# Optimization experiments

Measured on AMD Instinct MI355X. Metric: run time of the kernel, lower is better.

The kernel has to match this reference:

```python
import jax, jax.numpy as jnp
import numpy as np

COMMITMENT_COST = 0.25


def setup_inputs() -> dict:
    key = jax.random.key(0)
    k1, k2 = jax.random.split(key)
    B, S, D, V = 4, 1024, 1024, 32002
    inputs_embeds = jax.random.normal(k1, (B, S, D), dtype=jnp.float32)
    emb_weight = jax.random.normal(k2, (V, D), dtype=jnp.float32)
    attention_mask = jnp.ones((B, S), dtype=jnp.float32)
    return {
        "inputs_embeds": inputs_embeds,
        "emb_weight": emb_weight,
        "attention_mask": attention_mask,
        "lab_seq_len": 9,
    }


def reference(inputs_embeds, emb_weight, attention_mask, lab_seq_len):
    V, D = emb_weight.shape
    qn = (V - 2) // (lab_seq_len - 1)          # codes per segment
    nseg = lab_seq_len - 1                      # number of segments (V-2 divisible by qn)
    # codebook segments, skipping 2 special tokens: (nseg, qn, D)
    codes = emb_weight[2:2 + nseg * qn].reshape(nseg, qn, D)

    x = inputs_embeds.reshape(-1, D)            # (N, D)
    x2 = jnp.sum(x * x, axis=1)                 # (N,)
    c2 = jnp.sum(codes * codes, axis=-1)        # (nseg, qn)
    dots = jnp.einsum("nd,sqd->nsq", x, codes)  # (N, nseg, qn)
    dist = x2[:, None, None] + c2[None] - 2.0 * dots

    idx = jnp.argmin(dist, axis=-1)             # (N, nseg)
    # gather selected code per segment: (N, nseg, D)
    sel = codes[jnp.arange(nseg)[None, :], idx]
    # sum over segments then divide by segment count (matches torch loop + /j)
    quantized = jnp.mean(sel, axis=1).reshape(inputs_embeds.shape)

    mask = attention_mask[..., None]
    mse = jnp.mean((quantized * mask - inputs_embeds * mask) ** 2)
    # e_latent_loss and q_latent_loss are identical in the source
    loss = mse + COMMITMENT_COST * mse

    quantized_st = inputs_embeds + jax.lax.stop_gradient(quantized - inputs_embeds)
    return quantized_st, loss
```

## Files before the change

kernel.cpp:

```cpp
#include <hip/hip_runtime.h>
#include <stdint.h>

#define D_DIM  1024
#define NROWS  4096
#define NSEG   8
#define QN     4000
#define NCODES 32000
#define VOFF   2

#define BM 256
#define BN 256
#define BKI 128
#define LDK 40

#define MARGIN_BF 2.0f
#define MARGIN_I8 6.0f
#define CAP      262144u

#define C2_OFF     0u
#define X2_OFF     131072u
#define CELLS_OFF  147456u
#define MINF_OFF   409600u
#define CNT_OFF    540672u
#define PART_OFF   540928u
#define LIST_OFF   573696u
#define STASH_OFF  1622272u
#define WS_NEED_A  10010880u
#define XI8_OFF    10010880u
#define CI8_OFF    14205184u
#define SX_OFF     46973184u
#define SC_OFF     46989568u
#define WS_NEED_FAST 83935488u

typedef short bf16x8 __attribute__((ext_vector_type(8)));
typedef float f32x4  __attribute__((ext_vector_type(4)));
typedef int   i32x4  __attribute__((ext_vector_type(4)));

#define AS1(p) ((const __attribute__((address_space(1))) void*)(p))
#define AS3(p) ((__attribute__((address_space(3))) void*)(p))

__device__ inline unsigned short f2bs(float f) {
  unsigned u = __float_as_uint(f);
  unsigned r = (u + 0x7FFFu + ((u >> 16) & 1u)) >> 16;
  return (unsigned short)r;
}
__device__ inline unsigned shflx_u32(unsigned v, int m) {
  return (unsigned)__shfl_xor((int)v, m, 64);
}
__device__ inline unsigned packkey(float d, int qloc) {
  return (__float_as_uint(fmaxf(d, 0.0f)) & 0xFFFFFF80u) | (unsigned)qloc;
}

__global__ __launch_bounds__(256) void rowsq_kernel(const float* __restrict__ emb,
                                                    const float* __restrict__ x,
                                                    float* __restrict__ c2,
                                                    float* __restrict__ x2) {
  int b = blockIdx.x;
  int t = threadIdx.x;
  const float* src = (b < NCODES) ? (emb + (size_t)(VOFF + b) * D_DIM)
                                  : (x + (size_t)(b - NCODES) * D_DIM);
  float4 v = ((const float4*)src)[t];
  float s = v.x * v.x + v.y * v.y + v.z * v.z + v.w * v.w;
  for (int off = 32; off > 0; off >>= 1) s += __shfl_down(s, off, 64);
  __shared__ float red[4];
  if ((t & 63) == 0) red[t >> 6] = s;
  __syncthreads();
  if (t == 0) {
    float tot = red[0] + red[1] + red[2] + red[3];
    if (b < NCODES) c2[b] = tot; else x2[b - NCODES] = tot;
  }
}

__global__ __launch_bounds__(256) void convert_i8_kernel(const float* __restrict__ emb,
                                                         const float* __restrict__ x,
                                                         char* __restrict__ ci8,
                                                         char* __restrict__ xi8,
                                                         float* __restrict__ c2,
                                                         float* __restrict__ x2,
                                                         float* __restrict__ scs,
                                                         float* __restrict__ sxs) {
  int b = blockIdx.x;
  int t = threadIdx.x;
  const float* src;
  char* dst;
  if (b < NCODES) { src = emb + (size_t)(VOFF + b) * D_DIM; dst = ci8 + (size_t)b * D_DIM; }
  else            { src = x + (size_t)(b - NCODES) * D_DIM; dst = xi8 + (size_t)(b - NCODES) * D_DIM; }
  float4 v = ((const float4*)src)[t];
  float s = v.x * v.x + v.y * v.y + v.z * v.z + v.w * v.w;
  float a = fmaxf(fmaxf(fabsf(v.x), fabsf(v.y)), fmaxf(fabsf(v.z), fabsf(v.w)));
  for (int off = 32; off > 0; off >>= 1) {
    s += __shfl_down(s, off, 64);
    a = fmaxf(a, __shfl_down(a, off, 64));
  }
  __shared__ float redS[4], redA[4];
  if ((t & 63) == 0) { redS[t >> 6] = s; redA[t >> 6] = a; }
  __syncthreads();
  float amax = fmaxf(fmaxf(redA[0], redA[1]), fmaxf(redA[2], redA[3]));
  float inv = (amax > 0.0f) ? (127.0f / amax) : 0.0f;
  char4 o;
  o.x = (char)__float2int_rn(v.x * inv);
  o.y = (char)__float2int_rn(v.y * inv);
  o.z = (char)__float2int_rn(v.z * inv);
  o.w = (char)__float2int_rn(v.w * inv);
  ((char4*)dst)[t] = o;
  if (t == 0) {
    float tot = redS[0] + redS[1] + redS[2] + redS[3];
    float scale = amax * (1.0f / 127.0f);
    if (b < NCODES) { c2[b] = tot; scs[b] = scale; }
    else            { x2[b - NCODES] = tot; sxs[b - NCODES] = scale; }
  }
}

__global__ __launch_bounds__(512, 2) void score_i8_kernel(
    const char* __restrict__ xi8, const char* __restrict__ ci8,
    const float* __restrict__ c2, const float* __restrict__ x2,
    const float* __restrict__ scs, const float* __restrict__ sxs,
    unsigned* __restrict__ stash) {
  __shared__ char lA[2][BM][BKI];
  __shared__ char lB[2][BN][BKI];
  int tid = threadIdx.x;

  int bid = ((blockIdx.x & 7) << 8) | (blockIdx.x >> 3);
  int seg = bid >> 8;
  int lb  = bid & 255;
  int g   = lb >> 4;
  int gi  = lb & 15;
  int mx  = (g & 3) * 4 + (gi & 3);
  int qy  = (g >> 2) * 4 + (gi >> 2);
  int m0 = mx * BM, q0 = qy * BN;

  int lane = tid & 63, wid = tid >> 6;
  int wr = wid & 3, wc = wid >> 2;
  int lrow = lane & 15, kg = lane >> 4;
  const int co0 = ((kg       ^ (lrow & 7)) << 4);
  const int co1 = (((4 | kg) ^ (lrow & 7)) << 4);

  int csh = (((tid & 7) ^ ((tid >> 3) & 7)) << 4);
  const char* aSt = xi8 + (size_t)(m0 + (tid >> 3)) * D_DIM + csh;
  const char* bSt0; const char* bSt1; const char* bSt2; const char* bSt3;
  {
    int r0 = q0 +   0 + (tid >> 3); if (r0 > QN - 1) r0 = QN - 1;
    int r1 = q0 +  64 + (tid >> 3); if (r1 > QN - 1) r1 = QN - 1;
    int r2 = q0 + 128 + (tid >> 3); if (r2 > QN - 1) r2 = QN - 1;
    int r3 = q0 + 192 + (tid >> 3); if (r3 > QN - 1) r3 = QN - 1;
    bSt0 = ci8 + (size_t)(seg * QN + r0) * D_DIM + csh;
    bSt1 = ci8 + (size_t)(seg * QN + r1) * D_DIM + csh;
    bSt2 = ci8 + (size_t)(seg * QN + r2) * D_DIM + csh;
    bSt3 = ci8 + (size_t)(seg * QN + r3) * D_DIM + csh;
  }
  int ldsOff = tid << 4;

  i32x4 aR[2][2];
  i32x4 bR[4][2];
  i32x4 acc[4][8];
#pragma unroll
  for (int i = 0; i < 4; i++)
#pragma unroll
    for (int j = 0; j < 8; j++) acc[i][j] = (i32x4){0, 0, 0, 0};

#define STAGE_A(bb, kt) {                                                                      \
    __builtin_amdgcn_global_load_lds(AS1(aSt + (size_t)  0 * D_DIM + (kt)), AS3(&lA[bb][  0][0] + ldsOff), 16, 0, 0); \
    __builtin_amdgcn_global_load_lds(AS1(aSt + (size_t) 64 * D_DIM + (kt)), AS3(&lA[bb][ 64][0] + ldsOff), 16, 0, 0); \
    __builtin_amdgcn_global_load_lds(AS1(aSt + (size_t)128 * D_DIM + (kt)), AS3(&lA[bb][128][0] + ldsOff), 16, 0, 0); \
    __builtin_amdgcn_global_load_lds(AS1(aSt + (size_t)192 * D_DIM + (kt)), AS3(&lA[bb][192][0] + ldsOff), 16, 0, 0); }
#define STAGE_B(bb, kt) {                                                                      \
    __builtin_amdgcn_global_load_lds(AS1(bSt0 + (kt)), AS3(&lB[bb][  0][0] + ldsOff), 16, 0, 0); \
    __builtin_amdgcn_global_load_lds(AS1(bSt1 + (kt)), AS3(&lB[bb][ 64][0] + ldsOff), 16, 0, 0); \
    __builtin_amdgcn_global_load_lds(AS1(bSt2 + (kt)), AS3(&lB[bb][128][0] + ldsOff), 16, 0, 0); \
    __builtin_amdgcn_global_load_lds(AS1(bSt3 + (kt)), AS3(&lB[bb][192][0] + ldsOff), 16, 0, 0); }

#define READ_A(bb, mh) { _Pragma("unroll")                                         \
    for (int i = 0; i < 2; i++) {                                                  \
      const char* pa = &lA[bb][wr * 64 + (mh) * 32 + i * 16 + lrow][0];            \
      aR[i][0] = *(const i32x4*)(pa + co0);                                        \
      aR[i][1] = *(const i32x4*)(pa + co1); } }
#define READ_B(bb, nh) { _Pragma("unroll")                                         \
    for (int j = 0; j < 4; j++) {                                                  \
      const char* pb = &lB[bb][wc * 128 + (nh) * 64 + j * 16 + lrow][0];           \
      bR[j][0] = *(const i32x4*)(pb + co0);                                        \
      bR[j][1] = *(const i32x4*)(pb + co1); } }

#define MFMA_Q(mh, nh) {                                                           \
    __builtin_amdgcn_s_setprio(1);                                                 \
    _Pragma("unroll") for (int ks = 0; ks < 2; ks++)                               \
      _Pragma("unroll") for (int i = 0; i < 2; i++)                                \
        _Pragma("unroll") for (int j = 0; j < 4; j++)                              \
          acc[(mh)*2 + i][(nh)*4 + j] = __builtin_amdgcn_mfma_i32_16x16x64_i8(     \
              aR[i][ks], bR[j][ks], acc[(mh)*2 + i][(nh)*4 + j], 0, 0, 0);         \
    __builtin_amdgcn_s_setprio(0); }

#define VM0   asm volatile("s_waitcnt vmcnt(0)" ::: "memory")
#define LGKM0 asm volatile("s_waitcnt lgkmcnt(0)" ::: "memory")
#define BARX  __builtin_amdgcn_s_barrier()

  STAGE_A(0, 0);
  STAGE_B(0, 0);
  VM0; BARX;

  int buf = 0;
  for (int t = 0; t < 8; ++t) {
    int ktn = (t + 1) << 7;
    READ_A(buf, 0); READ_B(buf, 0);
    if (t < 7) STAGE_A(buf ^ 1, ktn);
    BARX; LGKM0; MFMA_Q(0, 0); BARX;
    READ_A(buf, 1);
    if (t < 7) STAGE_B(buf ^ 1, ktn);
    BARX; LGKM0; MFMA_Q(1, 0); BARX;
    READ_B(buf, 1);
    BARX; LGKM0; MFMA_Q(1, 1); BARX;
    READ_A(buf, 0);
    BARX; LGKM0; MFMA_Q(0, 1);
    VM0; LGKM0; BARX;
    buf ^= 1;
  }

  float c2v[8], s2c[8];
  bool  val[8];
#pragma unroll
  for (int nf = 0; nf < 8; nf++) {
    int q = q0 + wc * 128 + nf * 16 + lrow;
    val[nf] = (q < QN);
    int qc = val[nf] ? q : QN - 1;
    c2v[nf] = c2[seg * QN + qc];
    s2c[nf] = 2.0f * scs[seg * QN + qc];
  }

#pragma unroll
  for (int mf = 0; mf < 4; mf++) {
#pragma unroll
    for (int r = 0; r < 4; r++) {
      int grow = m0 + wr * 64 + mf * 16 + kg * 4 + r;
      float x2r = x2[grow];
      float sxr = sxs[grow];
      unsigned b1 = 0xFFFFFFFFu, b2 = 0xFFFFFFFFu;
#pragma unroll
      for (int nf = 0; nf < 8; nf++) {
        unsigned u = 0xFFFFFFFFu;
        if (val[nf]) {
          float d = (x2r + c2v[nf]) - sxr * s2c[nf] * (float)acc[mf][nf][r];
          u = packkey(d, nf * 16 + lrow);
        }
        if (u < b1) { b2 = b1; b1 = u; } else if (u < b2) b2 = u;
      }
#pragma unroll
      for (int m = 1; m < 16; m <<= 1) {
        unsigned o1 = shflx_u32(b1, m), o2 = shflx_u32(b2, m);
        unsigned n1 = min(b1, o1);
        unsigned n2 = min(max(b1, o1), min(b2, o2));
        b1 = n1; b2 = n2;
      }
      if (lrow == 0) {
        size_t base = ((size_t)(grow * NSEG + seg) * 32 + (qy * 2 + wc)) * 2;
        stash[base + 0] = b1;
        stash[base + 1] = b2;
      }
    }
  }
#undef STAGE_A
#undef STAGE_B
#undef READ_A
#undef READ_B
#undef MFMA_Q
#undef VM0
#undef LGKM0
#undef BARX
}

template<int MODE>
__global__ __launch_bounds__(256) void score_mfma_kernel(
    const float* __restrict__ x, const float* __restrict__ emb,
    const float* __restrict__ c2, const float* __restrict__ x2,
    unsigned* __restrict__ minf, unsigned* __restrict__ stash,
    unsigned* __restrict__ list, unsigned* __restrict__ cnt) {
  __shared__ short lA[2][128][LDK];
  __shared__ short lB[2][128][LDK];
  int tid = threadIdx.x;
  int m0 = blockIdx.x * 128, q0 = blockIdx.y * 128, seg = blockIdx.z;
  int lane = tid & 63, wid = tid >> 6;
  int wr = wid >> 1, wc = wid & 1;
  int lrow = lane & 15, kg = lane >> 4;

  int sr = tid >> 1;
  int kh = (tid & 1) << 4;
  const float* abase = x + (size_t)(m0 + sr) * D_DIM + kh;
  int qg = q0 + sr; if (qg > QN - 1) qg = QN - 1;
  const float* bbase = emb + (size_t)(VOFF + seg * QN + qg) * D_DIM + kh;

  f32x4 acc[4][4];
#pragma unroll
  for (int i = 0; i < 4; i++)
#pragma unroll
    for (int j = 0; j < 4; j++) acc[i][j] = (f32x4){0.f, 0.f, 0.f, 0.f};

  float4 ra0, ra1, ra2, ra3, rb0, rb1, rb2, rb3;

#define LOAD_TILE(kt) {                                          \
    const float4* ap = (const float4*)(abase + (kt));            \
    const float4* bp = (const float4*)(bbase + (kt));            \
    ra0 = ap[0]; ra1 = ap[1]; ra2 = ap[2]; ra3 = ap[3];          \
    rb0 = bp[0]; rb1 = bp[1]; rb2 = bp[2]; rb3 = bp[3]; }

#define WRITE_TILE(bb) {                                                       \
    bf16x8 p0, p1, q0v, q1v;                                                   \
    p0[0]=f2bs(ra0.x); p0[1]=f2bs(ra0.y); p0[2]=f2bs(ra0.z); p0[3]=f2bs(ra0.w);\
    p0[4]=f2bs(ra1.x); p0[5]=f2bs(ra1.y); p0[6]=f2bs(ra1.z); p0[7]=f2bs(ra1.w);\
    p1[0]=f2bs(ra2.x); p1[1]=f2bs(ra2.y); p1[2]=f2bs(ra2.z); p1[3]=f2bs(ra2.w);\
    p1[4]=f2bs(ra3.x); p1[5]=f2bs(ra3.y); p1[6]=f2bs(ra3.z); p1[7]=f2bs(ra3.w);\
    q0v[0]=f2bs(rb0.x); q0v[1]=f2bs(rb0.y); q0v[2]=f2bs(rb0.z); q0v[3]=f2bs(rb0.w);\
    q0v[4]=f2bs(rb1.x); q0v[5]=f2bs(rb1.y); q0v[6]=f2bs(rb1.z); q0v[7]=f2bs(rb1.w);\
    q1v[0]=f2bs(rb2.x); q1v[1]=f2bs(rb2.y); q1v[2]=f2bs(rb2.z); q1v[3]=f2bs(rb2.w);\
    q1v[4]=f2bs(rb3.x); q1v[5]=f2bs(rb3.y); q1v[6]=f2bs(rb3.z); q1v[7]=f2bs(rb3.w);\
    *(bf16x8*)&lA[bb][sr][kh]     = p0;  *(bf16x8*)&lA[bb][sr][kh + 8] = p1;   \
    *(bf16x8*)&lB[bb][sr][kh]     = q0v; *(bf16x8*)&lB[bb][sr][kh + 8] = q1v; }

#define COMPUTE(bb) {                                                              \
    bf16x8 af0 = *(const bf16x8*)&lA[bb][wr * 64 +  0 + lrow][kg * 8];             \
    bf16x8 af1 = *(const bf16x8*)&lA[bb][wr * 64 + 16 + lrow][kg * 8];             \
    bf16x8 af2 = *(const bf16x8*)&lA[bb][wr * 64 + 32 + lrow][kg * 8];             \
    bf16x8 af3 = *(const bf16x8*)&lA[bb][wr * 64 + 48 + lrow][kg * 8];             \
    bf16x8 bg0 = *(const bf16x8*)&lB[bb][wc * 64 +  0 + lrow][kg * 8];             \
    bf16x8 bg1 = *(const bf16x8*)&lB[bb][wc * 64 + 16 + lrow][kg * 8];             \
    bf16x8 bg2 = *(const bf16x8*)&lB[bb][wc * 64 + 32 + lrow][kg * 8];             \
    bf16x8 bg3 = *(const bf16x8*)&lB[bb][wc * 64 + 48 + lrow][kg * 8];             \
    acc[0][0] = __builtin_amdgcn_mfma_f32_16x16x32_bf16(af0, bg0, acc[0][0],0,0,0);\
    acc[0][1] = __builtin_amdgcn_mfma_f32_16x16x32_bf16(af0, bg1, acc[0][1],0,0,0);\
    acc[0][2] = __builtin_amdgcn_mfma_f32_16x16x32_bf16(af0, bg2, acc[0][2],0,0,0);\
    acc[0][3] = __builtin_amdgcn_mfma_f32_16x16x32_bf16(af0, bg3, acc[0][3],0,0,0);\
    acc[1][0] = __builtin_amdgcn_mfma_f32_16x16x32_bf16(af1, bg0, acc[1][0],0,0,0);\
    acc[1][1] = __builtin_amdgcn_mfma_f32_16x16x32_bf16(af1, bg1, acc[1][1],0,0,0);\
    acc[1][2] = __builtin_amdgcn_mfma_f32_16x16x32_bf16(af1, bg2, acc[1][2],0,0,0);\
    acc[1][3] = __builtin_amdgcn_mfma_f32_16x16x32_bf16(af1, bg3, acc[1][3],0,0,0);\
    acc[2][0] = __builtin_amdgcn_mfma_f32_16x16x32_bf16(af2, bg0, acc[2][0],0,0,0);\
    acc[2][1] = __builtin_amdgcn_mfma_f32_16x16x32_bf16(af2, bg1, acc[2][1],0,0,0);\
    acc[2][2] = __builtin_amdgcn_mfma_f32_16x16x32_bf16(af2, bg2, acc[2][2],0,0,0);\
    acc[2][3] = __builtin_amdgcn_mfma_f32_16x16x32_bf16(af2, bg3, acc[2][3],0,0,0);\
    acc[3][0] = __builtin_amdgcn_mfma_f32_16x16x32_bf16(af3, bg0, acc[3][0],0,0,0);\
    acc[3][1] = __builtin_amdgcn_mfma_f32_16x16x32_bf16(af3, bg1, acc[3][1],0,0,0);\
    acc[3][2] = __builtin_amdgcn_mfma_f32_16x16x32_bf16(af3, bg2, acc[3][2],0,0,0);\
    acc[3][3] = __builtin_amdgcn_mfma_f32_16x16x32_bf16(af3, bg3, acc[3][3],0,0,0); }

  LOAD_TILE(0);
  WRITE_TILE(0);
  __syncthreads();
  int buf = 0;
  for (int kt = 32; kt < D_DIM; kt += 32) {
    LOAD_TILE(kt);
    COMPUTE(buf);
    WRITE_TILE(buf ^ 1);
    __syncthreads();
    buf ^= 1;
  }
  COMPUTE(buf);
  unsigned* mbuf = (unsigned*)&lA[0][0][0];

  float c2v[4];
  bool  val[4];
  int   qloc[4];
#pragma unroll
  for (int nt = 0; nt < 4; nt++) {
    int ql = wc * 64 + nt * 16 + lrow;
    int q = q0 + ql;
    val[nt] = (q < QN);
    qloc[nt] = ql;
    c2v[nt] = c2[seg * QN + (val[nt] ? q : QN - 1)];
  }

#pragma unroll
  for (int mt = 0; mt < 4; mt++) {
#pragma unroll
    for (int r = 0; r < 4; r++) {
      int grow = m0 + wr * 64 + mt * 16 + kg * 4 + r;
      float x2r = x2[grow];
      if constexpr (MODE == 0) {
        float dmin = 1e30f;
#pragma unroll
        for (int nt = 0; nt < 4; nt++) {
          if (val[nt]) {
            float d = (x2r + c2v[nt]) - 2.0f * acc[mt][nt][r];
            dmin = fminf(dmin, d);
          }
        }
        dmin = fminf(dmin, __shfl_xor(dmin, 1, 64));
        dmin = fminf(dmin, __shfl_xor(dmin, 2, 64));
        dmin = fminf(dmin, __shfl_xor(dmin, 4, 64));
        dmin = fminf(dmin, __shfl_xor(dmin, 8, 64));
        if (lrow == 0)
          atomicMin(&minf[grow * NSEG + seg], __float_as_uint(fmaxf(dmin, 0.0f)));
      } else if constexpr (MODE == 1) {
        unsigned b1 = 0xFFFFFFFFu, b2 = 0xFFFFFFFFu;
#pragma unroll
        for (int nt = 0; nt < 4; nt++) {
          unsigned u = 0xFFFFFFFFu;
          if (val[nt]) {
            float d = (x2r + c2v[nt]) - 2.0f * acc[mt][nt][r];
            u = packkey(d, qloc[nt]);
          }
          if (u < b1) { b2 = b1; b1 = u; } else if (u < b2) b2 = u;
        }
#pragma unroll
        for (int m = 1; m < 16; m <<= 1) {
          unsigned o1 = shflx_u32(b1, m), o2 = shflx_u32(b2, m);
          unsigned n1 = min(b1, o1);
          unsigned n2 = min(max(b1, o1), min(b2, o2));
          b1 = n1; b2 = n2;
        }
        if (lrow == 0) {
          int rloc = wr * 64 + mt * 16 + kg * 4 + r;
          mbuf[(rloc * 2 + wc) * 2 + 0] = b1;
          mbuf[(rloc * 2 + wc) * 2 + 1] = b2;
        }
      } else {
        float dm = __uint_as_float(minf[grow * NSEG + seg]) + MARGIN_BF;
#pragma unroll
        for (int nt = 0; nt < 4; nt++) {
          if (val[nt]) {
            float d = (x2r + c2v[nt]) - 2.0f * acc[mt][nt][r];
            if (d <= dm) {
              unsigned idx = atomicAdd(cnt, 1u);
              if (idx < CAP)
                list[idx] = ((unsigned)grow << 15) | ((unsigned)seg << 12) |
                            (unsigned)(q0 + qloc[nt]);
            }
          }
        }
      }
    }
  }

  if constexpr (MODE == 1) {
    __syncthreads();
    if (tid < 128) {
      unsigned p1 = mbuf[(tid * 2 + 0) * 2 + 0];
      unsigned p2 = mbuf[(tid * 2 + 0) * 2 + 1];
      unsigned g1 = mbuf[(tid * 2 + 1) * 2 + 0];
      unsigned g2 = mbuf[(tid * 2 + 1) * 2 + 1];
      unsigned m1 = min(p1, g1);
      unsigned m2 = min(max(p1, g1), min(p2, g2));
      int grow = m0 + tid;
      size_t base = ((size_t)(grow * NSEG + seg) * 32 + blockIdx.y) * 2;
      stash[base + 0] = m1;
      stash[base + 1] = m2;
    }
  }
#undef LOAD_TILE
#undef WRITE_TILE
#undef COMPUTE
}

__global__ __launch_bounds__(256) void filter_rescore_kernel(
    const float* __restrict__ x, const float* __restrict__ emb,
    const float* __restrict__ c2, const float* __restrict__ x2,
    const unsigned* __restrict__ stash, unsigned long long* __restrict__ cells,
    float margin) {
  int cell = blockIdx.x * 4 + (threadIdx.x >> 6);
  int lane = threadIdx.x & 63;
  int row = cell >> 3, seg = cell & 7;
  unsigned e = stash[(size_t)cell * 64 + lane];
  unsigned m = e;
  for (int msk = 1; msk < 64; msk <<= 1) m = min(m, shflx_u32(m, msk));
  float dcut = __uint_as_float(m & 0xFFFFFF80u) + margin;
  int myq = ((lane >> 1) << 7) + (int)(e & 127u);
  bool qual = (e != 0xFFFFFFFFu) &&
              (__uint_as_float(e & 0xFFFFFF80u) <= dcut) && (myq < QN);
  unsigned long long mask = __ballot(qual);
  unsigned long long best = 0ULL;
  const float4* xr = (const float4*)(x + (size_t)row * D_DIM);
  float x2r = x2[row];
  while (mask) {
    int L = __ffsll((long long)mask) - 1;
    mask &= mask - 1;
    int q = __shfl(myq, L, 64);
    const float4* cr = (const float4*)(emb + (size_t)(VOFF + seg * QN + q) * D_DIM);
    float s = 0.f;
#pragma unroll
    for (int j = 0; j < 4; j++) {
      float4 a = xr[j * 64 + lane];
      float4 b = cr[j * 64 + lane];
      s += a.x * b.x + a.y * b.y + a.z * b.z + a.w * b.w;
    }
    for (int msk2 = 1; msk2 < 64; msk2 <<= 1) s += __shfl_xor(s, msk2, 64);
    float dist = (x2r + c2[seg * QN + q]) - 2.0f * s;
    unsigned u = __float_as_uint(dist);
    unsigned asc = (u & 0x80000000u) ? ~u : (u | 0x80000000u);
    unsigned long long p = ((unsigned long long)(~asc) << 32) |
                           (unsigned long long)(~(unsigned)q);
    if (p > best) best = p;
  }
  if (lane == 0) cells[(size_t)row * NSEG + seg] = best;
}

__global__ __launch_bounds__(256) void rescore_kernel(const float* __restrict__ x,
                                                      const float* __restrict__ emb,
                                                      const float* __restrict__ c2,
                                                      const float* __restrict__ x2,
                                                      const unsigned* __restrict__ list,
                                                      const unsigned* __restrict__ cnt,
                                                      unsigned long long* __restrict__ cells) {
  int nw = gridDim.x * 4;
  int wv = blockIdx.x * 4 + (threadIdx.x >> 6);
  int lane = threadIdx.x & 63;
  unsigned n = *cnt; if (n > CAP) n = CAP;
  for (unsigned i = wv; i < n; i += nw) {
    unsigned e = list[i];
    int row = e >> 15, seg = (e >> 12) & 7, q = e & 4095;
    const float4* xr = (const float4*)(x + (size_t)row * D_DIM);
    const float4* cr = (const float4*)(emb + (size_t)(VOFF + seg * QN + q) * D_DIM);
    float s = 0.f;
#pragma unroll
    for (int j = 0; j < 4; j++) {
      float4 a = xr[j * 64 + lane];
      float4 b = cr[j * 64 + lane];
      s += a.x * b.x + a.y * b.y + a.z * b.z + a.w * b.w;
    }
    for (int msk = 1; msk < 64; msk <<= 1) s += __shfl_xor(s, msk, 64);
    float dist = (x2[row] + c2[seg * QN + q]) - 2.0f * s;
    unsigned u = __float_as_uint(dist);
    unsigned asc = (u & 0x80000000u) ? ~u : (u | 0x80000000u);
    unsigned long long p = ((unsigned long long)(~asc) << 32) |
                           (unsigned long long)(~(unsigned)q);
    if (lane == 0) atomicMax(&cells[(size_t)row * NSEG + seg], p);
  }
}

__global__ __launch_bounds__(256) void gather_kernel(const float* __restrict__ x,
                                                     const float* __restrict__ emb,
                                                     const float* __restrict__ mask,
                                                     const unsigned long long* __restrict__ cells,
                                                     float* __restrict__ out,
                                                     double* __restrict__ part) {
  int n = blockIdx.x;
  int t = threadIdx.x;
  __shared__ int qsel[NSEG];
  if (t < NSEG) qsel[t] = (int)(~(unsigned)(cells[(size_t)n * NSEG + t] & 0xffffffffULL));
  __syncthreads();
  float4 xv = ((const float4*)(x + (size_t)n * D_DIM))[t];
  float ax = 0.f, ay = 0.f, az = 0.f, aw = 0.f;
#pragma unroll
  for (int s = 0; s < NSEG; s++) {
    float4 cv = ((const float4*)(emb + (size_t)(VOFF + s * QN + qsel[s]) * D_DIM))[t];
    ax += cv.x; ay += cv.y; az += cv.z; aw += cv.w;
  }
  float qx = ax * 0.125f, qy = ay * 0.125f, qz = az * 0.125f, qw = aw * 0.125f;
  float4 o4;
  o4.x = xv.x + (qx - xv.x);
  o4.y = xv.y + (qy - xv.y);
  o4.z = xv.z + (qz - xv.z);
  o4.w = xv.w + (qw - xv.w);
  ((float4*)(out + (size_t)n * D_DIM))[t] = o4;
  float mk = mask[n];
  float dx = qx * mk - xv.x * mk;
  float dy = qy * mk - xv.y * mk;
  float dz = qz * mk - xv.z * mk;
  float dw = qw * mk - xv.w * mk;
  float ss = dx * dx + dy * dy + dz * dz + dw * dw;
  double sd = (double)ss;
  for (int off = 32; off > 0; off >>= 1) sd += __shfl_down(sd, off, 64);
  __shared__ double red[4];
  if ((t & 63) == 0) red[t >> 6] = sd;
  __syncthreads();
  if (t == 0) part[n] = red[0] + red[1] + red[2] + red[3];
}

__global__ __launch_bounds__(256) void finalize_kernel(const double* __restrict__ part,
                                                       float* __restrict__ loss_out) {
  int t = threadIdx.x;
  double s = 0.0;
  for (int i = t; i < NROWS; i += 256) s += part[i];
  for (int off = 32; off > 0; off >>= 1) s += __shfl_down(s, off, 64);
  __shared__ double red[4];
  if ((t & 63) == 0) red[t >> 6] = s;
  __syncthreads();
  if (t == 0) {
    double tot = red[0] + red[1] + red[2] + red[3];
    float m = (float)(tot / (double)((size_t)NROWS * D_DIM));
    loss_out[0] = m + 0.25f * m;
  }
}

extern "C" void kernel_launch(void* const* d_in, const int* in_sizes, int n_in,
                              void* d_out, int out_size, void* d_ws, size_t ws_size,
                              hipStream_t stream) {
  const float* x    = (const float*)d_in[0];
  const float* emb  = (const float*)d_in[1];
  const float* mask = (const float*)d_in[2];
  (void)in_sizes; (void)n_in; (void)out_size;

  char* ws = (char*)d_ws;
  float* c2 = (float*)(ws + C2_OFF);
  float* x2 = (float*)(ws + X2_OFF);
  unsigned long long* cells = (unsigned long long*)(ws + CELLS_OFF);
  unsigned* minf = (unsigned*)(ws + MINF_OFF);
  unsigned* cnt  = (unsigned*)(ws + CNT_OFF);
  double*   part = (double*)(ws + PART_OFF);
  unsigned* list = (unsigned*)(ws + LIST_OFF);
  unsigned* stash = (unsigned*)(ws + STASH_OFF);
  char* xi8 = ws + XI8_OFF;
  char* ci8 = ws + CI8_OFF;
  float* sxs = (float*)(ws + SX_OFF);
  float* scs = (float*)(ws + SC_OFF);
  float* out = (float*)d_out;

  hipMemsetAsync(cells, 0, 262144, stream);
  hipMemsetAsync(cnt, 0, 256, stream);

  if (ws_size >= (size_t)WS_NEED_FAST) {
    convert_i8_kernel<<<dim3(NCODES + NROWS), 256, 0, stream>>>(emb, x, ci8, xi8, c2, x2, scs, sxs);
    score_i8_kernel<<<dim3(2048), 512, 0, stream>>>(xi8, ci8, c2, x2, scs, sxs, stash);
    filter_rescore_kernel<<<dim3(8192), 256, 0, stream>>>(x, emb, c2, x2, stash, cells, MARGIN_I8);
    gather_kernel<<<dim3(NROWS), 256, 0, stream>>>(x, emb, mask, cells, out, part);
  } else if (ws_size >= (size_t)WS_NEED_A) {
    rowsq_kernel<<<dim3(NCODES + NROWS), 256, 0, stream>>>(emb, x, c2, x2);
    score_mfma_kernel<1><<<dim3(NROWS / 128, (QN + 127) / 128, NSEG), 256, 0, stream>>>(
        x, emb, c2, x2, minf, stash, list, cnt);
    filter_rescore_kernel<<<dim3(8192), 256, 0, stream>>>(x, emb, c2, x2, stash, cells, MARGIN_BF);
    gather_kernel<<<dim3(NROWS), 256, 0, stream>>>(x, emb, mask, cells, out, part);
  } else {
    hipMemsetAsync(minf, 0xFF, 131072, stream);
    rowsq_kernel<<<dim3(NCODES + NROWS), 256, 0, stream>>>(emb, x, c2, x2);
    score_mfma_kernel<0><<<dim3(NROWS / 128, (QN + 127) / 128, NSEG), 256, 0, stream>>>(
        x, emb, c2, x2, minf, stash, list, cnt);
    score_mfma_kernel<2><<<dim3(NROWS / 128, (QN + 127) / 128, NSEG), 256, 0, stream>>>(
        x, emb, c2, x2, minf, stash, list, cnt);
    rescore_kernel<<<dim3(2048), 256, 0, stream>>>(x, emb, c2, x2, list, cnt, cells);
    gather_kernel<<<dim3(NROWS), 256, 0, stream>>>(x, emb, mask, cells, out, part);
  }
  finalize_kernel<<<dim3(1), 256, 0, stream>>>(part, out + (size_t)NROWS * D_DIM);
}
```

Measured before the change: 282.6 us.

## Retile int8 scoring GEMM to 128x128 blocks with triple-buffered K pipeline

The int8 distance-scoring kernel moves from 256x256 tiles with 512 threads and double buffering to 128x128 tiles with 256 threads, K steps of 64, and a three-stage global-to-LDS pipeline using partial vmcnt waits. The per-block top-2 results from the two wave columns are merged in shared memory before writing one stash entry per row, so the stash indexing changes to 32 column blocks of 128. The aim is better occupancy and load/compute overlap, at the cost of less data reuse per tile and four times as many blocks.

```diff
diff --git a/kernel.cpp b/kernel.cpp
--- a/kernel.cpp
+++ b/kernel.cpp
@@ -8,9 +8,6 @@
 #define NCODES 32000
 #define VOFF   2
 
-#define BM 256
-#define BN 256
-#define BKI 128
 #define LDK 40
 
 #define MARGIN_BF 2.0f
@@ -111,134 +108,128 @@
   }
 }
 
-__global__ __launch_bounds__(512, 2) void score_i8_kernel(
+__global__ __launch_bounds__(256) void score_i8_kernel(
     const char* __restrict__ xi8, const char* __restrict__ ci8,
     const float* __restrict__ c2, const float* __restrict__ x2,
     const float* __restrict__ scs, const float* __restrict__ sxs,
     unsigned* __restrict__ stash) {
-  __shared__ char lA[2][BM][BKI];
-  __shared__ char lB[2][BN][BKI];
+  __shared__ char lA[3][128][64];
+  __shared__ char lB[3][128][64];
   int tid = threadIdx.x;
 
-  int bid = ((blockIdx.x & 7) << 8) | (blockIdx.x >> 3);
-  int seg = bid >> 8;
-  int lb  = bid & 255;
-  int g   = lb >> 4;
-  int gi  = lb & 15;
-  int mx  = (g & 3) * 4 + (gi & 3);
-  int qy  = (g >> 2) * 4 + (gi >> 2);
-  int m0 = mx * BM, q0 = qy * BN;
+  int bid = ((blockIdx.x & 7) << 10) | (blockIdx.x >> 3);
+  int lb  = bid & 63;
+  int sb  = bid >> 6;
+  int smx = sb & 3;
+  int sqy = (sb >> 2) & 3;
+  int seg = sb >> 4;
+  int mx  = smx * 8 + (lb & 7);
+  int qy  = sqy * 8 + (lb >> 3);
+  int m0 = mx * 128, q0 = qy * 128;
 
   int lane = tid & 63, wid = tid >> 6;
-  int wr = wid & 3, wc = wid >> 2;
+  int wr = wid >> 1, wc = wid & 1;
   int lrow = lane & 15, kg = lane >> 4;
-  const int co0 = ((kg       ^ (lrow & 7)) << 4);
-  const int co1 = (((4 | kg) ^ (lrow & 7)) << 4);
-
-  int csh = (((tid & 7) ^ ((tid >> 3) & 7)) << 4);
-  const char* aSt = xi8 + (size_t)(m0 + (tid >> 3)) * D_DIM + csh;
-  const char* bSt0; const char* bSt1; const char* bSt2; const char* bSt3;
-  {
-    int r0 = q0 +   0 + (tid >> 3); if (r0 > QN - 1) r0 = QN - 1;
-    int r1 = q0 +  64 + (tid >> 3); if (r1 > QN - 1) r1 = QN - 1;
-    int r2 = q0 + 128 + (tid >> 3); if (r2 > QN - 1) r2 = QN - 1;
-    int r3 = q0 + 192 + (tid >> 3); if (r3 > QN - 1) r3 = QN - 1;
-    bSt0 = ci8 + (size_t)(seg * QN + r0) * D_DIM + csh;
-    bSt1 = ci8 + (size_t)(seg * QN + r1) * D_DIM + csh;
-    bSt2 = ci8 + (size_t)(seg * QN + r2) * D_DIM + csh;
-    bSt3 = ci8 + (size_t)(seg * QN + r3) * D_DIM + csh;
-  }
+  const int co = ((kg ^ ((lrow >> 1) & 3)) << 4);
+
+  int srow = tid >> 2;
+  int scol = (((tid & 3) ^ ((tid >> 3) & 3)) << 4);
+  const char* aSrc0 = xi8 + (size_t)(m0 + srow) * D_DIM + scol;
+  const char* aSrc1 = aSrc0 + (size_t)64 * D_DIM;
+  int qb0 = q0 + srow;      if (qb0 > QN - 1) qb0 = QN - 1;
+  int qb1 = q0 + srow + 64; if (qb1 > QN - 1) qb1 = QN - 1;
+  const char* bSrc0 = ci8 + (size_t)(seg * QN + qb0) * D_DIM + scol;
+  const char* bSrc1 = ci8 + (size_t)(seg * QN + qb1) * D_DIM + scol;
   int ldsOff = tid << 4;
 
-  i32x4 aR[2][2];
-  i32x4 bR[4][2];
-  i32x4 acc[4][8];
+  i32x4 acc[4][4];
 #pragma unroll
   for (int i = 0; i < 4; i++)
 #pragma unroll
-    for (int j = 0; j < 8; j++) acc[i][j] = (i32x4){0, 0, 0, 0};
-
-#define STAGE_A(bb, kt) {                                                                      \
-    __builtin_amdgcn_global_load_lds(AS1(aSt + (size_t)  0 * D_DIM + (kt)), AS3(&lA[bb][  0][0] + ldsOff), 16, 0, 0); \
-    __builtin_amdgcn_global_load_lds(AS1(aSt + (size_t) 64 * D_DIM + (kt)), AS3(&lA[bb][ 64][0] + ldsOff), 16, 0, 0); \
-    __builtin_amdgcn_global_load_lds(AS1(aSt + (size_t)128 * D_DIM + (kt)), AS3(&lA[bb][128][0] + ldsOff), 16, 0, 0); \
-    __builtin_amdgcn_global_load_lds(AS1(aSt + (size_t)192 * D_DIM + (kt)), AS3(&lA[bb][192][0] + ldsOff), 16, 0, 0); }
-#define STAGE_B(bb, kt) {                                                                      \
-    __builtin_amdgcn_global_load_lds(AS1(bSt0 + (kt)), AS3(&lB[bb][  0][0] + ldsOff), 16, 0, 0); \
-    __builtin_amdgcn_global_load_lds(AS1(bSt1 + (kt)), AS3(&lB[bb][ 64][0] + ldsOff), 16, 0, 0); \
-    __builtin_amdgcn_global_load_lds(AS1(bSt2 + (kt)), AS3(&lB[bb][128][0] + ldsOff), 16, 0, 0); \
-    __builtin_amdgcn_global_load_lds(AS1(bSt3 + (kt)), AS3(&lB[bb][192][0] + ldsOff), 16, 0, 0); }
-
-#define READ_A(bb, mh) { _Pragma("unroll")                                         \
-    for (int i = 0; i < 2; i++) {                                                  \
-      const char* pa = &lA[bb][wr * 64 + (mh) * 32 + i * 16 + lrow][0];            \
-      aR[i][0] = *(const i32x4*)(pa + co0);                                        \
-      aR[i][1] = *(const i32x4*)(pa + co1); } }
-#define READ_B(bb, nh) { _Pragma("unroll")                                         \
-    for (int j = 0; j < 4; j++) {                                                  \
-      const char* pb = &lB[bb][wc * 128 + (nh) * 64 + j * 16 + lrow][0];           \
-      bR[j][0] = *(const i32x4*)(pb + co0);                                        \
-      bR[j][1] = *(const i32x4*)(pb + co1); } }
-
-#define MFMA_Q(mh, nh) {                                                           \
+    for (int j = 0; j < 4; j++) acc[i][j] = (i32x4){0, 0, 0, 0};
+
+#define STAGE_F(bb, kt) {                                                            \
+    __builtin_amdgcn_global_load_lds(AS1(aSrc0 + (kt)), AS3(&lA[bb][0][0]  + ldsOff), 16, 0, 0); \
+    __builtin_amdgcn_global_load_lds(AS1(aSrc1 + (kt)), AS3(&lA[bb][64][0] + ldsOff), 16, 0, 0); \
+    __builtin_amdgcn_global_load_lds(AS1(bSrc0 + (kt)), AS3(&lB[bb][0][0]  + ldsOff), 16, 0, 0); \
+    __builtin_amdgcn_global_load_lds(AS1(bSrc1 + (kt)), AS3(&lB[bb][64][0] + ldsOff), 16, 0, 0); }
+
+#define COMPUTE_F(bb) {                                                            \
+    i32x4 af0 = *(const i32x4*)&lA[bb][wr * 64 +  0 + lrow][co];                   \
+    i32x4 af1 = *(const i32x4*)&lA[bb][wr * 64 + 16 + lrow][co];                   \
+    i32x4 af2 = *(const i32x4*)&lA[bb][wr * 64 + 32 + lrow][co];                   \
+    i32x4 af3 = *(const i32x4*)&lA[bb][wr * 64 + 48 + lrow][co];                   \
+    i32x4 bg0 = *(const i32x4*)&lB[bb][wc * 64 +  0 + lrow][co];                   \
+    i32x4 bg1 = *(const i32x4*)&lB[bb][wc * 64 + 16 + lrow][co];                   \
+    i32x4 bg2 = *(const i32x4*)&lB[bb][wc * 64 + 32 + lrow][co];                   \
+    i32x4 bg3 = *(const i32x4*)&lB[bb][wc * 64 + 48 + lrow][co];                   \
     __builtin_amdgcn_s_setprio(1);                                                 \
-    _Pragma("unroll") for (int ks = 0; ks < 2; ks++)                               \
-      _Pragma("unroll") for (int i = 0; i < 2; i++)                                \
-        _Pragma("unroll") for (int j = 0; j < 4; j++)                              \
-          acc[(mh)*2 + i][(nh)*4 + j] = __builtin_amdgcn_mfma_i32_16x16x64_i8(     \
-              aR[i][ks], bR[j][ks], acc[(mh)*2 + i][(nh)*4 + j], 0, 0, 0);         \
+    acc[0][0] = __builtin_amdgcn_mfma_i32_16x16x64_i8(af0, bg0, acc[0][0],0,0,0);  \
+    acc[0][1] = __builtin_amdgcn_mfma_i32_16x16x64_i8(af0, bg1, acc[0][1],0,0,0);  \
+    acc[0][2] = __builtin_amdgcn_mfma_i32_16x16x64_i8(af0, bg2, acc[0][2],0,0,0);  \
+    acc[0][3] = __builtin_amdgcn_mfma_i32_16x16x64_i8(af0, bg3, acc[0][3],0,0,0);  \
+    acc[1][0] = __builtin_amdgcn_mfma_i32_16x16x64_i8(af1, bg0, acc[1][0],0,0,0);  \
+    acc[1][1] = __builtin_amdgcn_mfma_i32_16x16x64_i8(af1, bg1, acc[1][1],0,0,0);  \
+    acc[1][2] = __builtin_amdgcn_mfma_i32_16x16x64_i8(af1, bg2, acc[1][2],0,0,0);  \
+    acc[1][3] = __builtin_amdgcn_mfma_i32_16x16x64_i8(af1, bg3, acc[1][3],0,0,0);  \
+    acc[2][0] = __builtin_amdgcn_mfma_i32_16x16x64_i8(af2, bg0, acc[2][0],0,0,0);  \
+    acc[2][1] = __builtin_amdgcn_mfma_i32_16x16x64_i8(af2, bg1, acc[2][1],0,0,0);  \
+    acc[2][2] = __builtin_amdgcn_mfma_i32_16x16x64_i8(af2, bg2, acc[2][2],0,0,0);  \
+    acc[2][3] = __builtin_amdgcn_mfma_i32_16x16x64_i8(af2, bg3, acc[2][3],0,0,0);  \
+    acc[3][0] = __builtin_amdgcn_mfma_i32_16x16x64_i8(af3, bg0, acc[3][0],0,0,0);  \
+    acc[3][1] = __builtin_amdgcn_mfma_i32_16x16x64_i8(af3, bg1, acc[3][1],0,0,0);  \
+    acc[3][2] = __builtin_amdgcn_mfma_i32_16x16x64_i8(af3, bg2, acc[3][2],0,0,0);  \
+    acc[3][3] = __builtin_amdgcn_mfma_i32_16x16x64_i8(af3, bg3, acc[3][3],0,0,0);  \
     __builtin_amdgcn_s_setprio(0); }
 
+#define VM4   asm volatile("s_waitcnt vmcnt(4)" ::: "memory")
 #define VM0   asm volatile("s_waitcnt vmcnt(0)" ::: "memory")
 #define LGKM0 asm volatile("s_waitcnt lgkmcnt(0)" ::: "memory")
 #define BARX  __builtin_amdgcn_s_barrier()
 
-  STAGE_A(0, 0);
-  STAGE_B(0, 0);
-  VM0; BARX;
-
-  int buf = 0;
-  for (int t = 0; t < 8; ++t) {
-    int ktn = (t + 1) << 7;
-    READ_A(buf, 0); READ_B(buf, 0);
-    if (t < 7) STAGE_A(buf ^ 1, ktn);
-    BARX; LGKM0; MFMA_Q(0, 0); BARX;
-    READ_A(buf, 1);
-    if (t < 7) STAGE_B(buf ^ 1, ktn);
-    BARX; LGKM0; MFMA_Q(1, 0); BARX;
-    READ_B(buf, 1);
-    BARX; LGKM0; MFMA_Q(1, 1); BARX;
-    READ_A(buf, 0);
-    BARX; LGKM0; MFMA_Q(0, 1);
-    VM0; LGKM0; BARX;
-    buf ^= 1;
-  }
-
-  float c2v[8], s2c[8];
-  bool  val[8];
-#pragma unroll
-  for (int nf = 0; nf < 8; nf++) {
-    int q = q0 + wc * 128 + nf * 16 + lrow;
-    val[nf] = (q < QN);
-    int qc = val[nf] ? q : QN - 1;
-    c2v[nf] = c2[seg * QN + qc];
-    s2c[nf] = 2.0f * scs[seg * QN + qc];
-  }
-
-#pragma unroll
-  for (int mf = 0; mf < 4; mf++) {
+  STAGE_F(0, 0);
+  STAGE_F(1, 64);
+  for (int tt = 0; tt < 12; tt += 3) {
+    VM4; LGKM0; BARX; STAGE_F(2, (tt + 2) * 64); COMPUTE_F(0);
+    VM4; LGKM0; BARX; STAGE_F(0, (tt + 3) * 64); COMPUTE_F(1);
+    VM4; LGKM0; BARX; STAGE_F(1, (tt + 4) * 64); COMPUTE_F(2);
+  }
+  VM4; LGKM0; BARX; STAGE_F(2, 14 * 64); COMPUTE_F(0);
+  VM4; LGKM0; BARX; STAGE_F(0, 15 * 64); COMPUTE_F(1);
+  VM4; LGKM0; BARX; COMPUTE_F(2);
+  VM0; LGKM0; BARX; COMPUTE_F(0);
+  __syncthreads();
+
+  unsigned* mbuf = (unsigned*)&lA[1][0][0];
+
+  float c2v[4], s2c[4];
+  bool  val[4];
+  int   qloc[4];
+#pragma unroll
+  for (int nt = 0; nt < 4; nt++) {
+    int ql = wc * 64 + nt * 16 + lrow;
+    int q = q0 + ql;
+    val[nt] = (q < QN);
+    qloc[nt] = ql;
+    int qc = val[nt] ? q : QN - 1;
+    c2v[nt] = c2[seg * QN + qc];
+    s2c[nt] = 2.0f * scs[seg * QN + qc];
+  }
+
+#pragma unroll
+  for (int mt = 0; mt < 4; mt++) {
 #pragma unroll
     for (int r = 0; r < 4; r++) {
-      int grow = m0 + wr * 64 + mf * 16 + kg * 4 + r;
+      int grow = m0 + wr * 64 + mt * 16 + kg * 4 + r;
       float x2r = x2[grow];
       float sxr = sxs[grow];
       unsigned b1 = 0xFFFFFFFFu, b2 = 0xFFFFFFFFu;
 #pragma unroll
-      for (int nf = 0; nf < 8; nf++) {
+      for (int nt = 0; nt < 4; nt++) {
         unsigned u = 0xFFFFFFFFu;
-        if (val[nf]) {
-          float d = (x2r + c2v[nf]) - sxr * s2c[nf] * (float)acc[mf][nf][r];
-          u = packkey(d, nf * 16 + lrow);
+        if (val[nt]) {
+          float d = (x2r + c2v[nt]) - sxr * s2c[nt] * (float)acc[mt][nt][r];
+          u = packkey(d, qloc[nt]);
         }
         if (u < b1) { b2 = b1; b1 = u; } else if (u < b2) b2 = u;
       }
@@ -250,17 +241,28 @@
         b1 = n1; b2 = n2;
       }
       if (lrow == 0) {
-        size_t base = ((size_t)(grow * NSEG + seg) * 32 + (qy * 2 + wc)) * 2;
-        stash[base + 0] = b1;
-        stash[base + 1] = b2;
+        int rloc = wr * 64 + mt * 16 + kg * 4 + r;
+        mbuf[(rloc * 2 + wc) * 2 + 0] = b1;
+        mbuf[(rloc * 2 + wc) * 2 + 1] = b2;
       }
     }
   }
-#undef STAGE_A
-#undef STAGE_B
-#undef READ_A
-#undef READ_B
-#undef MFMA_Q
+  __syncthreads();
+  if (tid < 128) {
+    unsigned p1 = mbuf[(tid * 2 + 0) * 2 + 0];
+    unsigned p2 = mbuf[(tid * 2 + 0) * 2 + 1];
+    unsigned g1 = mbuf[(tid * 2 + 1) * 2 + 0];
+    unsigned g2 = mbuf[(tid * 2 + 1) * 2 + 1];
+    unsigned m1 = min(p1, g1);
+    unsigned m2 = min(max(p1, g1), min(p2, g2));
+    int grow = m0 + tid;
+    size_t base = ((size_t)(grow * NSEG + seg) * 32 + qy) * 2;
+    stash[base + 0] = m1;
+    stash[base + 1] = m2;
+  }
+#undef STAGE_F
+#undef COMPUTE_F
+#undef VM4
 #undef VM0
 #undef LGKM0
 #undef BARX
@@ -605,7 +607,7 @@
 
   if (ws_size >= (size_t)WS_NEED_FAST) {
     convert_i8_kernel<<<dim3(NCODES + NROWS), 256, 0, stream>>>(emb, x, ci8, xi8, c2, x2, scs, sxs);
-    score_i8_kernel<<<dim3(2048), 512, 0, stream>>>(xi8, ci8, c2, x2, scs, sxs, stash);
+    score_i8_kernel<<<dim3(8192), 256, 0, stream>>>(xi8, ci8, c2, x2, scs, sxs, stash);
     filter_rescore_kernel<<<dim3(8192), 256, 0, stream>>>(x, emb, c2, x2, stash, cells, MARGIN_I8);
     gather_kernel<<<dim3(NROWS), 256, 0, stream>>>(x, emb, mask, cells, out, part);
   } else if (ws_size >= (size_t)WS_NEED_A) {
```

Result: slower. 333.8 us (+18.1%).
